# Kernel optimization log

Hardware: AMD Instinct MI355X
Metric: run time of the kernel (lower is better)

The kernel has to match this reference:

```python
import jax, jax.numpy as jnp
import numpy as np

EMB_DIM = 64
B, S, D = 64, 1024, 64

def setup_inputs() -> dict:
    key = jax.random.key(0)
    k1, k2, k3, k4, k5 = jax.random.split(key, 5)
    return {
        "query": jax.random.normal(k1, (B, S, D), dtype=jnp.float32),
        "key": jax.random.normal(k2, (B, S, D), dtype=jnp.float32),
        "value": jax.random.normal(k3, (B, S, D), dtype=jnp.float32),
        "a_key": jax.random.normal(k4, (S, S, D), dtype=jnp.float32),
        "a_value": jax.random.normal(k5, (S, S, D), dtype=jnp.float32),
    }

def reference(query, key, value, a_key, a_value):
    scale = jnp.sqrt(jnp.asarray(EMB_DIM, dtype=query.dtype))
    # standard content-content scores: [B, Sq, Sk]
    qk = jnp.einsum("bqd,bkd->bqk", query, key)
    # relative key scores: a_key is [Sq, Sk, D]; contract over D per query position
    rel_qk = jnp.einsum("bqd,qkd->bqk", query, a_key)
    attn = jax.nn.softmax((qk + rel_qk) / scale, axis=-1)
    # content values + relative values
    qkv = jnp.einsum("bqk,bkd->bqd", attn, value)
    rel_qkv = jnp.einsum("bqk,qkd->bqd", attn, a_value)
    return qkv + rel_qkv, attn
```

## Files before the change

### kernel.cpp

```cpp
#include <hip/hip_runtime.h>
#include <stdint.h>

#define S_ 1024
#define D_ 64
#define B_ 64

typedef short short8 __attribute__((ext_vector_type(8)));
typedef unsigned short ushort8 __attribute__((ext_vector_type(8)));
typedef float f32x4 __attribute__((ext_vector_type(4)));

__device__ __forceinline__ unsigned short f2bf(float x) {
    uint32_t u = __builtin_bit_cast(uint32_t, x);
    return (unsigned short)((u + 0x7FFFu + ((u >> 16) & 1u)) >> 16);
}
__device__ __forceinline__ float bf2f(unsigned short b) {
    return __builtin_bit_cast(float, ((uint32_t)b) << 16);
}
__device__ __forceinline__ uint32_t pack2(float a, float b) {
    return (uint32_t)f2bf(a) | ((uint32_t)f2bf(b) << 16);
}
__device__ __forceinline__ short8 mkfrag(float4 a, float4 b) {
    union { short8 s; uint32_t u[4]; } r;
    r.u[0] = pack2(a.x, a.y); r.u[1] = pack2(a.z, a.w);
    r.u[2] = pack2(b.x, b.y); r.u[3] = pack2(b.z, b.w);
    return r.s;
}
__device__ __forceinline__ int scidx(int row, int k) {
    return (((row << 10) + (k & ~7)) ^ ((row & 15) << 3)) + (k & 7);
}

__global__ __launch_bounds__(256) void k1_qk(const float* __restrict__ Q,
                                             const float* __restrict__ Kk,
                                             float* __restrict__ qk) {
    __shared__ __align__(16) unsigned short Qs[128][72];
    __shared__ __align__(16) unsigned short Ks[128][72];
    const float SCL = 0.18033688011112042f;
    const int bx = blockIdx.x;
    const int b  = bx >> 6;
    const int q0 = ((bx >> 3) & 7) << 7;
    const int k0 = (bx & 7) << 7;
    const int t  = threadIdx.x;
#pragma unroll
    for (int i = 0; i < 8; ++i) {
        int f = (i << 8) + t;
        int row = f >> 4, c = (f & 15) << 2;
        float4 v = *reinterpret_cast<const float4*>(&Q[((size_t)(b * S_ + q0 + row) << 6) + c]);
        *reinterpret_cast<uint2*>(&Qs[row][c]) = make_uint2(pack2(v.x, v.y), pack2(v.z, v.w));
        float4 u = *reinterpret_cast<const float4*>(&Kk[((size_t)(b * S_ + k0 + row) << 6) + c]);
        *reinterpret_cast<uint2*>(&Ks[row][c]) = make_uint2(pack2(u.x, u.y), pack2(u.z, u.w));
    }
    __syncthreads();
    const int l = t & 63, w = t >> 6, lr = l & 15, lg = l >> 4;
    short8 a[2][2];
#pragma unroll
    for (int mi = 0; mi < 2; ++mi)
#pragma unroll
        for (int h = 0; h < 2; ++h)
            a[mi][h] = *reinterpret_cast<const short8*>(&Qs[((w * 2 + mi) << 4) + lr][h * 32 + lg * 8]);
    f32x4 acc[2][8] = {};
#pragma unroll
    for (int n = 0; n < 8; ++n) {
        short8 b0 = *reinterpret_cast<const short8*>(&Ks[(n << 4) + lr][lg * 8]);
        short8 b1 = *reinterpret_cast<const short8*>(&Ks[(n << 4) + lr][32 + lg * 8]);
#pragma unroll
        for (int mi = 0; mi < 2; ++mi) {
            acc[mi][n] = __builtin_amdgcn_mfma_f32_16x16x32_bf16(a[mi][0], b0, acc[mi][n], 0, 0, 0);
            acc[mi][n] = __builtin_amdgcn_mfma_f32_16x16x32_bf16(a[mi][1], b1, acc[mi][n], 0, 0, 0);
        }
    }
#pragma unroll
    for (int mi = 0; mi < 2; ++mi)
#pragma unroll
        for (int n = 0; n < 8; ++n)
#pragma unroll
            for (int r = 0; r < 4; ++r) {
                int qq = q0 + ((w * 2 + mi) << 4) + (lg << 2) + r;
                int kc = k0 + (n << 4) + lr;
                qk[((size_t)(b * S_ + qq) << 10) + kc] = acc[mi][n][r] * SCL;
            }
}

__device__ __forceinline__ void tpose_store_p(unsigned short* Tls, int pitch, float4 p,
                                              int kb, int t) {
    const int l = t & 63, lr = l & 15, lg = l >> 4;
    float v0 = p.x, v1 = p.y, v2 = p.z, v3 = p.w;
    float y0 = __shfl_xor(v0, 16), y1 = __shfl_xor(v1, 16),
          y2 = __shfl_xor(v2, 16), y3 = __shfl_xor(v3, 16);
    bool o = (lg & 1);
    float n0 = o ? y1 : v0, n1 = o ? v1 : y0, n2 = o ? y3 : v2, n3 = o ? v3 : y2;
    float z0 = __shfl_xor(n0, 32), z1 = __shfl_xor(n1, 32),
          z2 = __shfl_xor(n2, 32), z3 = __shfl_xor(n3, 32);
    bool h = (lg & 2);
    float T0 = h ? z2 : n0, T1 = h ? z3 : n1, T2 = h ? n2 : z0, T3 = h ? n3 : z1;
    int d = (lr << 2) + lg;
    *reinterpret_cast<uint2*>(&Tls[d * pitch + kb]) = make_uint2(pack2(T0, T1), pack2(T2, T3));
}

__global__ __launch_bounds__(1024) void k2_mid(const float* __restrict__ Q,
                                               const float* __restrict__ AK,
                                               const float* __restrict__ AV,
                                               float* __restrict__ attn,
                                               float* __restrict__ outp) {
    __shared__ __align__(16) unsigned short Sc[64 * 1024];
    __shared__ __align__(16) unsigned short Qs[64][72];
    __shared__ __align__(16) unsigned short Ak[2][64][72];
    __shared__ float invs[64];
    const float SCL = 0.18033688011112042f;
    const int q = blockIdx.x;
    const int t = threadIdx.x;
    const int l = t & 63, w = t >> 6, lr = l & 15, lg = l >> 4;
    const int wq = w & 3;
    const int wg = w >> 2;
    const int srow = t >> 4, c4 = (t & 15) << 2;

    {
        const float* qp = &Q[((size_t)(srow * S_ + q) << 6) + c4];
        float4 a = *reinterpret_cast<const float4*>(qp);
        *reinterpret_cast<uint2*>(&Qs[srow][c4]) =
            make_uint2(pack2(a.x * SCL, a.y * SCL), pack2(a.z * SCL, a.w * SCL));
    }
    __syncthreads();
    short8 qa[4][2];
#pragma unroll
    for (int bh = 0; bh < 4; ++bh)
#pragma unroll
        for (int h = 0; h < 2; ++h)
            qa[bh][h] = *reinterpret_cast<const short8*>(
                &Qs[(bh << 4) + lr][(h << 5) + (lg << 3)]);

    {
        const float* base = &AK[((size_t)q << 16) + (((wq << 4) + lr) << 6) + (lg << 3)];
        float4 A0[2], A1[2], A2[2], A3[2];
#define LDA(buf, i4) do { const float* p_ = base + ((size_t)((wg << 2) + (i4)) << 12); \
        A0[buf] = *reinterpret_cast<const float4*>(p_);                                \
        A1[buf] = *reinterpret_cast<const float4*>(p_ + 4);                            \
        A2[buf] = *reinterpret_cast<const float4*>(p_ + 32);                           \
        A3[buf] = *reinterpret_cast<const float4*>(p_ + 36); } while (0)
        LDA(0, 0); LDA(1, 1);
#pragma unroll 2
        for (int i4 = 0; i4 < 4; ++i4) {
            const int buf = i4 & 1;
            short8 ak0 = mkfrag(A0[buf], A1[buf]);
            short8 ak1 = mkfrag(A2[buf], A3[buf]);
            if (i4 < 2) LDA(buf, i4 + 2);
            int kbase = (((wg << 2) + i4) << 6) + (wq << 4) + (lg << 2);
#pragma unroll
            for (int bh = 0; bh < 4; ++bh) {
                f32x4 c = {};
                c = __builtin_amdgcn_mfma_f32_16x16x32_bf16(ak0, qa[bh][0], c, 0, 0, 0);
                c = __builtin_amdgcn_mfma_f32_16x16x32_bf16(ak1, qa[bh][1], c, 0, 0, 0);
                *reinterpret_cast<uint2*>(&Sc[scidx((bh << 4) + lr, kbase)]) =
                    make_uint2(pack2(c[0], c[1]), pack2(c[2], c[3]));
            }
        }
#undef LDA
    }
    __syncthreads();

    const float* avbase = &AV[(size_t)q << 16];
    float4 pv[2];
#pragma unroll
    for (int s = 0; s < 2; ++s)
        pv[s] = *reinterpret_cast<const float4*>(
            &avbase[((size_t)s << 12) + ((size_t)srow << 6) + c4]);

    {
        const int ch = t & 15;
        const float* qkrow = &attn[((size_t)(srow * S_ + q) << 10)];
        float s = 0.f;
#pragma unroll 4
        for (int i = 0; i < 8; ++i) {
            int k = (((i << 4) + ch) << 3);
            float4 g0 = *reinterpret_cast<const float4*>(&qkrow[k]);
            float4 g1 = *reinterpret_cast<const float4*>(&qkrow[k + 4]);
            int idx = scidx(srow, k);
            ushort8 rel = *reinterpret_cast<const ushort8*>(&Sc[idx]);
            float p0 = exp2f(g0.x + bf2f(rel[0]));
            float p1 = exp2f(g0.y + bf2f(rel[1]));
            float p2 = exp2f(g0.z + bf2f(rel[2]));
            float p3 = exp2f(g0.w + bf2f(rel[3]));
            float p4 = exp2f(g1.x + bf2f(rel[4]));
            float p5 = exp2f(g1.y + bf2f(rel[5]));
            float p6 = exp2f(g1.z + bf2f(rel[6]));
            float p7 = exp2f(g1.w + bf2f(rel[7]));
            s += ((p0 + p1) + (p2 + p3)) + ((p4 + p5) + (p6 + p7));
            ushort8 e;
            e[0] = f2bf(p0); e[1] = f2bf(p1); e[2] = f2bf(p2); e[3] = f2bf(p3);
            e[4] = f2bf(p4); e[5] = f2bf(p5); e[6] = f2bf(p6); e[7] = f2bf(p7);
            *reinterpret_cast<ushort8*>(&Sc[idx]) = e;
        }
        s += __shfl_xor(s, 1); s += __shfl_xor(s, 2);
        s += __shfl_xor(s, 4); s += __shfl_xor(s, 8);
        if (ch == 0) invs[srow] = 1.0f / s;
    }
    __syncthreads();

    tpose_store_p(&Ak[0][0][0], 72, pv[0], (w << 2), t);
    __syncthreads();

    f32x4 oacc = {};
#pragma unroll 2
    for (int tt = 0; tt < 16; ++tt) {
        const int cur = tt & 1, nxt = cur ^ 1;
        short8 bb0 = *reinterpret_cast<const short8*>(&Ak[cur][(wq << 4) + lr][lg << 3]);
        short8 bb1 = *reinterpret_cast<const short8*>(&Ak[cur][(wq << 4) + lr][32 + (lg << 3)]);
        if (tt < 15) tpose_store_p(&Ak[nxt][0][0], 72, pv[nxt], (w << 2), t);
        if (tt < 14)
            pv[cur] = *reinterpret_cast<const float4*>(
                &avbase[((size_t)(tt + 2) << 12) + ((size_t)srow << 6) + c4]);
        {
            int col = (t & 255) << 2;
            int row = (tt << 2) + (t >> 8);
            uint2 u = *reinterpret_cast<const uint2*>(&Sc[scidx(row, col)]);
            float inv = invs[row];
            float4 o = make_float4(bf2f((unsigned short)(u.x & 0xffff)) * inv,
                                   bf2f((unsigned short)(u.x >> 16)) * inv,
                                   bf2f((unsigned short)(u.y & 0xffff)) * inv,
                                   bf2f((unsigned short)(u.y >> 16)) * inv);
            *reinterpret_cast<float4*>(&attn[((size_t)(row * S_ + q) << 10) + col]) = o;
        }
        short8 ea0 = *reinterpret_cast<const short8*>(
            &Sc[scidx((wg << 4) + lr, (tt << 6) + (lg << 3))]);
        short8 ea1 = *reinterpret_cast<const short8*>(
            &Sc[scidx((wg << 4) + lr, (tt << 6) + 32 + (lg << 3))]);
        oacc = __builtin_amdgcn_mfma_f32_16x16x32_bf16(ea0, bb0, oacc, 0, 0, 0);
        oacc = __builtin_amdgcn_mfma_f32_16x16x32_bf16(ea1, bb1, oacc, 0, 0, 0);
        __syncthreads();
    }
#pragma unroll
    for (int r = 0; r < 4; ++r) {
        int brow = (wg << 4) + (lg << 2) + r;
        outp[((size_t)(brow * S_ + q) << 6) + (wq << 4) + lr] = oacc[r] * invs[brow];
    }
}

__global__ __launch_bounds__(1024) void k3_pv(const float* __restrict__ V,
                                              const float* __restrict__ attn,
                                              float* __restrict__ outp) {
    __shared__ __align__(16) unsigned short Vt[64 * 1032];
    const int b  = blockIdx.x >> 2;
    const int qq = blockIdx.x & 3;
    const int t  = threadIdx.x;
    const int l = t & 63, w = t >> 6, lr = l & 15, lg = l >> 4;
    const int wq = w & 3;
    const int dh = (w >> 2) & 1;
    const int qg = w >> 3;

    for (int kt = 0; kt < 16; ++kt) {
        float4 pvv = *reinterpret_cast<const float4*>(
            &V[((size_t)(b * S_ + (kt << 6) + (t >> 4)) << 6) + ((t & 15) << 2)]);
        tpose_store_p(&Vt[0], 1032, pvv, (kt << 6) + (w << 2), t);
    }
    __syncthreads();

#pragma unroll
    for (int qs2 = 0; qs2 < 2; ++qs2) {
        const int qs = (qg << 1) + qs2;
        const float* arow = &attn[((size_t)((b * S_ + (qq << 8) + (qs << 6) + (wq << 4) + lr)) << 10) + (lg << 3)];
        float4 A0[2], A1[2], A2[2], A3[2];
#define LDP(buf, kt) do { const float* p_ = arow + ((kt) << 6);        \
        A0[buf] = *reinterpret_cast<const float4*>(p_);                \
        A1[buf] = *reinterpret_cast<const float4*>(p_ + 4);            \
        A2[buf] = *reinterpret_cast<const float4*>(p_ + 32);           \
        A3[buf] = *reinterpret_cast<const float4*>(p_ + 36); } while (0)
        LDP(0, 0); LDP(1, 1);
        f32x4 acc[2] = {};
#pragma unroll 2
        for (int kt = 0; kt < 16; ++kt) {
            const int buf = kt & 1;
            short8 a0 = mkfrag(A0[buf], A1[buf]);
            short8 a1 = mkfrag(A2[buf], A3[buf]);
            if (kt < 14) LDP(buf, kt + 2);
#pragma unroll
            for (int n = 0; n < 2; ++n) {
                const unsigned short* vb = &Vt[((dh << 5) + (n << 4) + lr) * 1032 + (kt << 6) + (lg << 3)];
                short8 b0 = *reinterpret_cast<const short8*>(vb);
                short8 b1 = *reinterpret_cast<const short8*>(vb + 32);
                acc[n] = __builtin_amdgcn_mfma_f32_16x16x32_bf16(a0, b0, acc[n], 0, 0, 0);
                acc[n] = __builtin_amdgcn_mfma_f32_16x16x32_bf16(a1, b1, acc[n], 0, 0, 0);
            }
        }
#undef LDP
#pragma unroll
        for (int n = 0; n < 2; ++n)
#pragma unroll
            for (int r = 0; r < 4; ++r) {
                size_t idx = ((size_t)(b * S_ + (qq << 8) + (qs << 6) + (wq << 4) + (lg << 2) + r) << 6)
                             + (dh << 5) + (n << 4) + lr;
                outp[idx] += acc[n][r];
            }
    }
}

extern "C" void kernel_launch(void* const* d_in, const int* in_sizes, int n_in,
                              void* d_out, int out_size, void* d_ws, size_t ws_size,
                              hipStream_t stream) {
    (void)in_sizes; (void)n_in; (void)out_size; (void)d_ws; (void)ws_size;
    const float* Q  = (const float*)d_in[0];
    const float* K  = (const float*)d_in[1];
    const float* V  = (const float*)d_in[2];
    const float* AK = (const float*)d_in[3];
    const float* AV = (const float*)d_in[4];
    float* outp = (float*)d_out;
    float* attn = outp + (size_t)B_ * S_ * D_;

    k1_qk <<<dim3(64 * 8 * 8), dim3(256),  0, stream>>>(Q, K, attn);
    k2_mid<<<dim3(1024),       dim3(1024), 0, stream>>>(Q, AK, AV, attn, outp);
    k3_pv <<<dim3(256),        dim3(1024), 0, stream>>>(V, attn, outp);
}
```

Measured before the change: 424.8 us.

## Fuse qk score add and exp into the rel-score MFMA, bf16 workspace for qk

```diff
diff --git a/kernel.cpp b/kernel.cpp
--- a/kernel.cpp
+++ b/kernel.cpp
@@ -8,12 +8,13 @@
 typedef short short8 __attribute__((ext_vector_type(8)));
 typedef unsigned short ushort8 __attribute__((ext_vector_type(8)));
 typedef float f32x4 __attribute__((ext_vector_type(4)));
-
-__device__ __forceinline__ unsigned short f2bf(float x) {
+typedef unsigned short u16;
+
+__device__ __forceinline__ u16 f2bf(float x) {
     uint32_t u = __builtin_bit_cast(uint32_t, x);
-    return (unsigned short)((u + 0x7FFFu + ((u >> 16) & 1u)) >> 16);
-}
-__device__ __forceinline__ float bf2f(unsigned short b) {
+    return (u16)((u + 0x7FFFu + ((u >> 16) & 1u)) >> 16);
+}
+__device__ __forceinline__ float bf2f(u16 b) {
     return __builtin_bit_cast(float, ((uint32_t)b) << 16);
 }
 __device__ __forceinline__ uint32_t pack2(float a, float b) {
@@ -29,11 +30,13 @@
     return (((row << 10) + (k & ~7)) ^ ((row & 15) << 3)) + (k & 7);
 }
 
+template <int WS>
 __global__ __launch_bounds__(256) void k1_qk(const float* __restrict__ Q,
                                              const float* __restrict__ Kk,
-                                             float* __restrict__ qk) {
-    __shared__ __align__(16) unsigned short Qs[128][72];
-    __shared__ __align__(16) unsigned short Ks[128][72];
+                                             float* __restrict__ qkf,
+                                             u16* __restrict__ qkb) {
+    __shared__ __align__(16) u16 Qs[128][72];
+    __shared__ __align__(16) u16 Ks[128][72];
     const float SCL = 0.18033688011112042f;
     const int bx = blockIdx.x;
     const int b  = bx >> 6;
@@ -76,11 +79,13 @@
             for (int r = 0; r < 4; ++r) {
                 int qq = q0 + ((w * 2 + mi) << 4) + (lg << 2) + r;
                 int kc = k0 + (n << 4) + lr;
-                qk[((size_t)(b * S_ + qq) << 10) + kc] = acc[mi][n][r] * SCL;
+                size_t idx = ((size_t)(b * S_ + qq) << 10) + kc;
+                if (WS) qkb[idx] = f2bf(acc[mi][n][r] * SCL);
+                else    qkf[idx] = acc[mi][n][r] * SCL;
             }
 }
 
-__device__ __forceinline__ void tpose_store_p(unsigned short* Tls, int pitch, float4 p,
+__device__ __forceinline__ void tpose_store_p(u16* Tls, int pitch, float4 p,
                                               int kb, int t) {
     const int l = t & 63, lr = l & 15, lg = l >> 4;
     float v0 = p.x, v1 = p.y, v2 = p.z, v3 = p.w;
@@ -96,22 +101,26 @@
     *reinterpret_cast<uint2*>(&Tls[d * pitch + kb]) = make_uint2(pack2(T0, T1), pack2(T2, T3));
 }
 
+template <int WS>
 __global__ __launch_bounds__(1024) void k2_mid(const float* __restrict__ Q,
                                                const float* __restrict__ AK,
                                                const float* __restrict__ AV,
+                                               const u16* __restrict__ qkb,
+                                               const float* __restrict__ qkf,
                                                float* __restrict__ attn,
                                                float* __restrict__ outp) {
-    __shared__ __align__(16) unsigned short Sc[64 * 1024];
-    __shared__ __align__(16) unsigned short Qs[64][72];
-    __shared__ __align__(16) unsigned short Ak[2][64][72];
+    __shared__ __align__(16) u16 Sc[64 * 1024];
+    __shared__ __align__(16) u16 Qs[64][72];
+    __shared__ __align__(16) u16 Ak[2][64][72];
     __shared__ float invs[64];
-    const float SCL = 0.18033688011112042f;
+    float* partials = reinterpret_cast<float*>(&Ak[0][0][0]);
     const int q = blockIdx.x;
     const int t = threadIdx.x;
     const int l = t & 63, w = t >> 6, lr = l & 15, lg = l >> 4;
     const int wq = w & 3;
     const int wg = w >> 2;
     const int srow = t >> 4, c4 = (t & 15) << 2;
+    const float SCL = 0.18033688011112042f;
 
     {
         const float* qp = &Q[((size_t)(srow * S_ + q) << 6) + c4];
@@ -128,70 +137,77 @@
             qa[bh][h] = *reinterpret_cast<const short8*>(
                 &Qs[(bh << 4) + lr][(h << 5) + (lg << 3)]);
 
+    float slocal[4] = {};
     {
         const float* base = &AK[((size_t)q << 16) + (((wq << 4) + lr) << 6) + (lg << 3)];
         float4 A0[2], A1[2], A2[2], A3[2];
+        uint2  cb[2][4];
+        float4 cf[2][4];
 #define LDA(buf, i4) do { const float* p_ = base + ((size_t)((wg << 2) + (i4)) << 12); \
         A0[buf] = *reinterpret_cast<const float4*>(p_);                                \
         A1[buf] = *reinterpret_cast<const float4*>(p_ + 4);                            \
         A2[buf] = *reinterpret_cast<const float4*>(p_ + 32);                           \
         A3[buf] = *reinterpret_cast<const float4*>(p_ + 36); } while (0)
-        LDA(0, 0); LDA(1, 1);
+#define LDC(buf, i4) do {                                                              \
+        int k0_ = ((((wg << 2) + (i4)) << 6)) + (wq << 4) + (lg << 2);                 \
+        _Pragma("unroll")                                                              \
+        for (int bh_ = 0; bh_ < 4; ++bh_) {                                            \
+            size_t ci_ = ((size_t)(((bh_ << 4) + lr) * S_ + q) << 10) + k0_;           \
+            if (WS) cb[buf][bh_] = *reinterpret_cast<const uint2*>(&qkb[ci_]);         \
+            else    cf[buf][bh_] = *reinterpret_cast<const float4*>(&qkf[ci_]);        \
+        } } while (0)
+        LDA(0, 0); LDC(0, 0); LDA(1, 1); LDC(1, 1);
 #pragma unroll 2
         for (int i4 = 0; i4 < 4; ++i4) {
             const int buf = i4 & 1;
             short8 ak0 = mkfrag(A0[buf], A1[buf]);
             short8 ak1 = mkfrag(A2[buf], A3[buf]);
-            if (i4 < 2) LDA(buf, i4 + 2);
             int kbase = (((wg << 2) + i4) << 6) + (wq << 4) + (lg << 2);
 #pragma unroll
             for (int bh = 0; bh < 4; ++bh) {
-                f32x4 c = {};
+                f32x4 c;
+                if (WS) {
+                    uint2 cu = cb[buf][bh];
+                    c[0] = bf2f((u16)(cu.x & 0xffff));
+                    c[1] = bf2f((u16)(cu.x >> 16));
+                    c[2] = bf2f((u16)(cu.y & 0xffff));
+                    c[3] = bf2f((u16)(cu.y >> 16));
+                } else {
+                    float4 cu = cf[buf][bh];
+                    c[0] = cu.x; c[1] = cu.y; c[2] = cu.z; c[3] = cu.w;
+                }
                 c = __builtin_amdgcn_mfma_f32_16x16x32_bf16(ak0, qa[bh][0], c, 0, 0, 0);
                 c = __builtin_amdgcn_mfma_f32_16x16x32_bf16(ak1, qa[bh][1], c, 0, 0, 0);
+                float p0 = exp2f(c[0]), p1 = exp2f(c[1]),
+                      p2 = exp2f(c[2]), p3 = exp2f(c[3]);
+                slocal[bh] += (p0 + p1) + (p2 + p3);
                 *reinterpret_cast<uint2*>(&Sc[scidx((bh << 4) + lr, kbase)]) =
-                    make_uint2(pack2(c[0], c[1]), pack2(c[2], c[3]));
+                    make_uint2(pack2(p0, p1), pack2(p2, p3));
             }
+            if (i4 < 2) { LDA(buf, i4 + 2); LDC(buf, i4 + 2); }
         }
 #undef LDA
-    }
-    __syncthreads();
-
+#undef LDC
+    }
+#pragma unroll
+    for (int bh = 0; bh < 4; ++bh) {
+        float s2 = slocal[bh];
+        s2 += __shfl_xor(s2, 16);
+        s2 += __shfl_xor(s2, 32);
+        if (lg == 0) partials[(w << 6) + (bh << 4) + lr] = s2;
+    }
     const float* avbase = &AV[(size_t)q << 16];
     float4 pv[2];
 #pragma unroll
     for (int s = 0; s < 2; ++s)
         pv[s] = *reinterpret_cast<const float4*>(
             &avbase[((size_t)s << 12) + ((size_t)srow << 6) + c4]);
-
-    {
-        const int ch = t & 15;
-        const float* qkrow = &attn[((size_t)(srow * S_ + q) << 10)];
+    __syncthreads();
+    if (t < 64) {
         float s = 0.f;
-#pragma unroll 4
-        for (int i = 0; i < 8; ++i) {
-            int k = (((i << 4) + ch) << 3);
-            float4 g0 = *reinterpret_cast<const float4*>(&qkrow[k]);
-            float4 g1 = *reinterpret_cast<const float4*>(&qkrow[k + 4]);
-            int idx = scidx(srow, k);
-            ushort8 rel = *reinterpret_cast<const ushort8*>(&Sc[idx]);
-            float p0 = exp2f(g0.x + bf2f(rel[0]));
-            float p1 = exp2f(g0.y + bf2f(rel[1]));
-            float p2 = exp2f(g0.z + bf2f(rel[2]));
-            float p3 = exp2f(g0.w + bf2f(rel[3]));
-            float p4 = exp2f(g1.x + bf2f(rel[4]));
-            float p5 = exp2f(g1.y + bf2f(rel[5]));
-            float p6 = exp2f(g1.z + bf2f(rel[6]));
-            float p7 = exp2f(g1.w + bf2f(rel[7]));
-            s += ((p0 + p1) + (p2 + p3)) + ((p4 + p5) + (p6 + p7));
-            ushort8 e;
-            e[0] = f2bf(p0); e[1] = f2bf(p1); e[2] = f2bf(p2); e[3] = f2bf(p3);
-            e[4] = f2bf(p4); e[5] = f2bf(p5); e[6] = f2bf(p6); e[7] = f2bf(p7);
-            *reinterpret_cast<ushort8*>(&Sc[idx]) = e;
-        }
-        s += __shfl_xor(s, 1); s += __shfl_xor(s, 2);
-        s += __shfl_xor(s, 4); s += __shfl_xor(s, 8);
-        if (ch == 0) invs[srow] = 1.0f / s;
+#pragma unroll
+        for (int w2 = 0; w2 < 16; ++w2) s += partials[(w2 << 6) + t];
+        invs[t] = 1.0f / s;
     }
     __syncthreads();
 
@@ -213,10 +229,10 @@
             int row = (tt << 2) + (t >> 8);
             uint2 u = *reinterpret_cast<const uint2*>(&Sc[scidx(row, col)]);
             float inv = invs[row];
-            float4 o = make_float4(bf2f((unsigned short)(u.x & 0xffff)) * inv,
-                                   bf2f((unsigned short)(u.x >> 16)) * inv,
-                                   bf2f((unsigned short)(u.y & 0xffff)) * inv,
-                                   bf2f((unsigned short)(u.y >> 16)) * inv);
+            float4 o = make_float4(bf2f((u16)(u.x & 0xffff)) * inv,
+                                   bf2f((u16)(u.x >> 16)) * inv,
+                                   bf2f((u16)(u.y & 0xffff)) * inv,
+                                   bf2f((u16)(u.y >> 16)) * inv);
             *reinterpret_cast<float4*>(&attn[((size_t)(row * S_ + q) << 10) + col]) = o;
         }
         short8 ea0 = *reinterpret_cast<const short8*>(
@@ -237,7 +253,7 @@
 __global__ __launch_bounds__(1024) void k3_pv(const float* __restrict__ V,
                                               const float* __restrict__ attn,
                                               float* __restrict__ outp) {
-    __shared__ __align__(16) unsigned short Vt[64 * 1032];
+    __shared__ __align__(16) u16 Vt[64 * 1032];
     const int b  = blockIdx.x >> 2;
     const int qq = blockIdx.x & 3;
     const int t  = threadIdx.x;
@@ -273,7 +289,7 @@
             if (kt < 14) LDP(buf, kt + 2);
 #pragma unroll
             for (int n = 0; n < 2; ++n) {
-                const unsigned short* vb = &Vt[((dh << 5) + (n << 4) + lr) * 1032 + (kt << 6) + (lg << 3)];
+                const u16* vb = &Vt[((dh << 5) + (n << 4) + lr) * 1032 + (kt << 6) + (lg << 3)];
                 short8 b0 = *reinterpret_cast<const short8*>(vb);
                 short8 b1 = *reinterpret_cast<const short8*>(vb + 32);
                 acc[n] = __builtin_amdgcn_mfma_f32_16x16x32_bf16(a0, b0, acc[n], 0, 0, 0);
@@ -295,7 +311,7 @@
 extern "C" void kernel_launch(void* const* d_in, const int* in_sizes, int n_in,
                               void* d_out, int out_size, void* d_ws, size_t ws_size,
                               hipStream_t stream) {
-    (void)in_sizes; (void)n_in; (void)out_size; (void)d_ws; (void)ws_size;
+    (void)in_sizes; (void)n_in; (void)out_size;
     const float* Q  = (const float*)d_in[0];
     const float* K  = (const float*)d_in[1];
     const float* V  = (const float*)d_in[2];
@@ -303,8 +319,15 @@
     const float* AV = (const float*)d_in[4];
     float* outp = (float*)d_out;
     float* attn = outp + (size_t)B_ * S_ * D_;
-
-    k1_qk <<<dim3(64 * 8 * 8), dim3(256),  0, stream>>>(Q, K, attn);
-    k2_mid<<<dim3(1024),       dim3(1024), 0, stream>>>(Q, AK, AV, attn, outp);
-    k3_pv <<<dim3(256),        dim3(1024), 0, stream>>>(V, attn, outp);
-}
+    u16*   qkb  = (u16*)d_ws;
+    const size_t qk_bytes = (size_t)B_ * S_ * S_ * sizeof(u16);
+
+    if (ws_size >= qk_bytes) {
+        k1_qk<1><<<dim3(64 * 8 * 8), dim3(256),  0, stream>>>(Q, K, attn, qkb);
+        k2_mid<1><<<dim3(1024),      dim3(1024), 0, stream>>>(Q, AK, AV, qkb, attn, attn, outp);
+    } else {
+        k1_qk<0><<<dim3(64 * 8 * 8), dim3(256),  0, stream>>>(Q, K, attn, qkb);
+        k2_mid<0><<<dim3(1024),      dim3(1024), 0, stream>>>(Q, AK, AV, qkb, attn, attn, outp);
+    }
+    k3_pv<<<dim3(256), dim3(1024), 0, stream>>>(V, attn, outp);
+}
```

After: 456.6 us. +7.5%, slower.
